# Kernel tuning notes

Hardware: AMD Instinct MI355X
Metric: run time of the kernel (lower is better)

## Reference

```python
import jax, jax.numpy as jnp
import numpy as np

I, H, B, T = 512, 1024, 64, 256

def _lstm_cell(x, h, c, Wih, Whh, bih, bhh):
    # PyTorch LSTMCell: gates ordered (i, f, g, o)
    g = x @ Wih.T + h @ Whh.T + (bih + bhh)
    i, f, gc, o = jnp.split(g, 4, axis=-1)
    i = jax.nn.sigmoid(i)
    f = jax.nn.sigmoid(f)
    gc = jnp.tanh(gc)
    o = jax.nn.sigmoid(o)
    c_new = f * c + i * gc
    return o * jnp.tanh(c_new), c_new

def setup_inputs() -> dict:
    key = jax.random.key(0)
    ks = jax.random.split(key, 20)
    s = 0.05
    d = {"x": jax.random.normal(ks[0], (B, T, I), dtype=jnp.float32)}
    # cell1: input I; cells 2-4: input H
    ins = [I, H, H, H]
    k = 1
    for n in range(1, 5):
        d[f"Wih{n}"] = jax.random.normal(ks[k], (4 * H, ins[n - 1]), dtype=jnp.float32) * s; k += 1
        d[f"Whh{n}"] = jax.random.normal(ks[k], (4 * H, H), dtype=jnp.float32) * s; k += 1
        d[f"bih{n}"] = jax.random.normal(ks[k], (4 * H,), dtype=jnp.float32) * s; k += 1
        d[f"bhh{n}"] = jax.random.normal(ks[k], (4 * H,), dtype=jnp.float32) * s; k += 1
    return d

def _mtrnn(x, Wih1, Whh1, bih1, bhh1, Wih2, Whh2, bih2, bhh2,
           Wih3, Whh3, bih3, bhh3, Wih4, Whh4, bih4, bhh4):
    b = x.shape[0]
    z = jnp.zeros((b, H), dtype=x.dtype)
    init = (z, z, z, z, z, z, z, z)

    def step(carry, inp):
        x_t, t = inp
        h1, c1, h2, c2, h3, c3, h4, c4 = carry
        h1, c1 = _lstm_cell(x_t, h1, c1, Wih1, Whh1, bih1, bhh1)
        nh2, nc2 = _lstm_cell(h1, h2, c2, Wih2, Whh2, bih2, bhh2)
        m2 = (t % 2 == 0)
        h2 = jnp.where(m2, nh2, h2); c2 = jnp.where(m2, nc2, c2)
        nh3, nc3 = _lstm_cell(h2, h3, c3, Wih3, Whh3, bih3, bhh3)
        m3 = (t % 4 == 0)
        h3 = jnp.where(m3, nh3, h3); c3 = jnp.where(m3, nc3, c3)
        nh4, nc4 = _lstm_cell(h3, h4, c4, Wih4, Whh4, bih4, bhh4)
        m4 = (t % 8 == 0)
        h4 = jnp.where(m4, nh4, h4); c4 = jnp.where(m4, nc4, c4)
        return (h1, c1, h2, c2, h3, c3, h4, c4), None

    xs = (jnp.transpose(x, (1, 0, 2)), jnp.arange(x.shape[1]))  # time-major scan
    (h1, c1, h2, c2, h3, c3, h4, c4), _ = jax.lax.scan(step, init, xs)
    return h4

def reference(x, Wih1, Whh1, bih1, bhh1, Wih2, Whh2, bih2, bhh2,
              Wih3, Whh3, bih3, bhh3, Wih4, Whh4, bih4, bhh4):
    return _mtrnn(x, Wih1, Whh1, bih1, bhh1, Wih2, Whh2, bih2, bhh2,
                  Wih3, Whh3, bih3, bhh3, Wih4, Whh4, bih4, bhh4)
```

## Files before the change

kernel.cpp:

```cpp
#include <hip/hip_runtime.h>

using u16 = unsigned short;
typedef short bf16x8 __attribute__((ext_vector_type(8)));
typedef float f32x4 __attribute__((ext_vector_type(4)));

static constexpr size_t OFF_W1  = 0;
static constexpr size_t OFF_W2  = OFF_W1 + (size_t)4096*1536*2;
static constexpr size_t OFF_W3  = OFF_W2 + (size_t)4096*2048*2;
static constexpr size_t OFF_W4  = OFF_W3 + (size_t)4096*2048*2;
static constexpr size_t OFF_BS  = OFF_W4 + (size_t)4096*2048*2;
static constexpr size_t OFF_XB  = OFF_BS + (size_t)4*4096*4;
static constexpr size_t OFF_H   = OFF_XB + (size_t)256*64*512*2;
static constexpr size_t OFF_C   = OFF_H  + (size_t)4*2*65536*2;
static constexpr size_t OFF_BAR = OFF_C  + (size_t)4*65536*4;
static constexpr size_t WS_TOTAL= OFF_BAR + 4096;

__device__ __forceinline__ u16 f2b(float f) {
  union { float f; unsigned u; } a; a.f = f;
  unsigned r = a.u + 0x7fffu + ((a.u >> 16) & 1u);
  return (u16)(r >> 16);
}

__global__ void k_prep_cell(const float* __restrict__ Wih, const float* __restrict__ Whh,
                            int Kih, int Khh, u16* __restrict__ Wcat)
{
  const int r = blockIdx.y;
  const int k = blockIdx.x * blockDim.x + threadIdx.x;
  const int K = Kih + Khh;
  float v = (k < Kih) ? Wih[(size_t)r * Kih + k] : Whh[(size_t)r * Khh + (k - Kih)];
  Wcat[(size_t)r * K + k] = f2b(v);
}

__global__ void k_bsum(const float* b1i, const float* b1h, const float* b2i, const float* b2h,
                       const float* b3i, const float* b3h, const float* b4i, const float* b4h,
                       float* __restrict__ bs)
{
  const int i = blockIdx.x * blockDim.x + threadIdx.x;
  const int n = i >> 12, j = i & 4095;
  const float* bi = (n == 0) ? b1i : (n == 1) ? b2i : (n == 2) ? b3i : b4i;
  const float* bh = (n == 0) ? b1h : (n == 1) ? b2h : (n == 2) ? b3h : b4h;
  bs[i] = bi[j] + bh[j];
}

__global__ void k_xconv(const float* __restrict__ x, u16* __restrict__ xb)
{
  const int blk = blockIdx.x;
  const int t = blk >> 6, b = blk & 63;
  const int i = threadIdx.x * 4;
  const float4 v = *(const float4*)(x + ((size_t)b * 256 + t) * 512 + i);
  ushort4 s;
  s.x = f2b(v.x); s.y = f2b(v.y); s.z = f2b(v.z); s.w = f2b(v.w);
  *(ushort4*)(xb + (size_t)blk * 512 + i) = s;
}

__global__ void k_zero(uint4* __restrict__ p, int n16)
{
  const int i = blockIdx.x * blockDim.x + threadIdx.x;
  if (i < n16) { uint4 z; z.x = z.y = z.z = z.w = 0u; p[i] = z; }
}

__device__ __forceinline__ void grid_barrier(unsigned* bar, unsigned gen)
{
  __syncthreads();
  if (threadIdx.x == 0) {
    unsigned* gcnt = bar + ((blockIdx.x & 7) << 5);
    unsigned* root = bar + 256;
    unsigned* rel  = bar + 288;
    const unsigned p = __hip_atomic_fetch_add(gcnt, 1u, __ATOMIC_ACQ_REL, __HIP_MEMORY_SCOPE_AGENT);
    if (p == gen * 16u + 15u) {
      const unsigned q = __hip_atomic_fetch_add(root, 1u, __ATOMIC_ACQ_REL, __HIP_MEMORY_SCOPE_AGENT);
      if (q == gen * 8u + 7u)
        __hip_atomic_store(rel, gen + 1u, __ATOMIC_RELEASE, __HIP_MEMORY_SCOPE_AGENT);
    }
    while (__hip_atomic_load(rel, __ATOMIC_ACQUIRE, __HIP_MEMORY_SCOPE_AGENT) < gen + 1u)
      __builtin_amdgcn_s_sleep(2);
  }
  __syncthreads();
}

template<int NSEC>
__device__ __forceinline__ void run_cell(
    char* A_lds, float (*gl)[32][17],
    const u16* const (&src)[NSEC], const int (&sstr)[NSEC], const int (&soff)[NSEC],
    const u16* __restrict__ Wc, const int Kw,
    const float* __restrict__ bsum, float* __restrict__ cst,
    u16* __restrict__ hnext, float* __restrict__ outp,
    const int rh, const int cg)
{
  const int tid  = threadIdx.x;
  const int lane = tid & 63;
  const int wv   = tid >> 6;
  const int l15  = lane & 15;
  const int l4   = lane >> 4;
  const int xr   = (l15 & 7) << 4;

  f32x4 acc0 = {0.f, 0.f, 0.f, 0.f};
  f32x4 acc1 = {0.f, 0.f, 0.f, 0.f};

  const size_t wrow = (size_t)((wv << 10) + (cg << 4) + l15) * (size_t)Kw + (l4 << 3);

  uint4 wA[16], wB[16];
  {
    const u16* wr = Wc + wrow;
    #pragma unroll
    for (int k0 = 0; k0 < 16; ++k0) wA[k0] = *(const uint4*)(wr + (k0 << 5));
  }

  #pragma unroll
  for (int s = 0; s < NSEC; ++s) {
    __syncthreads();
    {
      const u16* S = src[s];
      const int st = sstr[s];
      const int so = soff[s];
      #pragma unroll
      for (int i = 0; i < 8; ++i) {
        const int ch = tid + (i << 8);
        const int lr = ch >> 6;
        const int kc = (ch & 63) << 3;
        const uint4 v = *(const uint4*)(S + (size_t)(rh * 32 + lr) * st + so + kc);
        *(uint4*)(A_lds + lr * 1024 + ((kc * 2) ^ ((lr & 7) << 4))) = v;
      }
    }
    if (s + 1 < NSEC) {
      const u16* wr = Wc + wrow + ((s + 1) << 9);
      if ((s & 1) == 0) {
        #pragma unroll
        for (int k0 = 0; k0 < 16; ++k0) wB[k0] = *(const uint4*)(wr + (k0 << 5));
      } else {
        #pragma unroll
        for (int k0 = 0; k0 < 16; ++k0) wA[k0] = *(const uint4*)(wr + (k0 << 5));
      }
    }
    __syncthreads();
    const uint4* wc = ((s & 1) == 0) ? wA : wB;
    #pragma unroll
    for (int k0 = 0; k0 < 16; ++k0) {
      const int kb = (k0 << 6) + (l4 << 4);
      bf16x8 a0 = *(const bf16x8*)(A_lds + (l15 << 10) + (kb ^ xr));
      bf16x8 a1 = *(const bf16x8*)(A_lds + ((16 + l15) << 10) + (kb ^ xr));
      bf16x8 b  = __builtin_bit_cast(bf16x8, wc[k0]);
      acc0 = __builtin_amdgcn_mfma_f32_16x16x32_bf16(a0, b, acc0, 0, 0, 0);
      acc1 = __builtin_amdgcn_mfma_f32_16x16x32_bf16(a1, b, acc1, 0, 0, 0);
    }
  }

  __syncthreads();
  #pragma unroll
  for (int r = 0; r < 4; ++r) {
    gl[wv][(l4 << 2) + r][l15]      = acc0[r];
    gl[wv][16 + (l4 << 2) + r][l15] = acc1[r];
  }
  __syncthreads();

  for (int e = tid; e < 512; e += 256) {
    const int lr = e >> 4, lc = e & 15;
    const int col  = (cg << 4) + lc;
    const int brow = rh * 32 + lr;
    const float gi = gl[0][lr][lc] + bsum[col];
    const float gf = gl[1][lr][lc] + bsum[1024 + col];
    const float gg = gl[2][lr][lc] + bsum[2048 + col];
    const float go = gl[3][lr][lc] + bsum[3072 + col];
    const float ii = 1.f / (1.f + __expf(-gi));
    const float ff = 1.f / (1.f + __expf(-gf));
    const float gc = tanhf(gg);
    const float oo = 1.f / (1.f + __expf(-go));
    const int idx = (brow << 10) + col;
    const float cn = ff * cst[idx] + ii * gc;
    cst[idx] = cn;
    const float hn = oo * tanhf(cn);
    hnext[idx] = f2b(hn);
    if (outp) outp[idx] = hn;
  }
}

__global__ void __launch_bounds__(256) k_mtrnn(char* __restrict__ ws, float* __restrict__ out)
{
  __shared__ alignas(16) char A_lds[32768];
  __shared__ float gl[4][32][17];

  const int bid = blockIdx.x;
  const int rh  = bid & 1;
  const int cg  = bid >> 1;

  const u16* W1 = (const u16*)(ws + OFF_W1);
  const u16* W2 = (const u16*)(ws + OFF_W2);
  const u16* W3 = (const u16*)(ws + OFF_W3);
  const u16* W4 = (const u16*)(ws + OFF_W4);
  const float* bs = (const float*)(ws + OFF_BS);
  const u16* xb = (const u16*)(ws + OFF_XB);
  u16* hb       = (u16*)(ws + OFF_H);
  float* cs     = (float*)(ws + OFF_C);
  unsigned* bar = (unsigned*)(ws + OFF_BAR);

  #define HBUF(n, p) (hb + (((n) * 2 + (p)) << 16))

  unsigned gen = 0;
  int c1 = 0, c2 = 0, c3 = 0, c4 = 0;

  #pragma unroll 1
  for (int t = 0; t < 256; ++t) {
    {
      const u16* xt = xb + (size_t)t * 32768;
      const u16* h1 = HBUF(0, c1);
      const u16* src[3] = { xt, h1, h1 };
      const int sstr[3] = { 512, 1024, 1024 };
      const int soff[3] = { 0, 0, 512 };
      run_cell<3>(A_lds, gl, src, sstr, soff, W1, 1536, bs, cs,
                  HBUF(0, c1 ^ 1), nullptr, rh, cg);
      c1 ^= 1;
      grid_barrier(bar, gen); ++gen;
    }
    if ((t & 1) == 0) {
      const u16* hi = HBUF(0, c1);
      const u16* hs = HBUF(1, c2);
      const u16* src[4] = { hi, hi, hs, hs };
      const int sstr[4] = { 1024, 1024, 1024, 1024 };
      const int soff[4] = { 0, 512, 0, 512 };
      run_cell<4>(A_lds, gl, src, sstr, soff, W2, 2048, bs + 4096, cs + 65536,
                  HBUF(1, c2 ^ 1), nullptr, rh, cg);
      c2 ^= 1;
      grid_barrier(bar, gen); ++gen;
    }
    if ((t & 3) == 0) {
      const u16* hi = HBUF(1, c2);
      const u16* hs = HBUF(2, c3);
      const u16* src[4] = { hi, hi, hs, hs };
      const int sstr[4] = { 1024, 1024, 1024, 1024 };
      const int soff[4] = { 0, 512, 0, 512 };
      run_cell<4>(A_lds, gl, src, sstr, soff, W3, 2048, bs + 8192, cs + 131072,
                  HBUF(2, c3 ^ 1), nullptr, rh, cg);
      c3 ^= 1;
      grid_barrier(bar, gen); ++gen;
    }
    if ((t & 7) == 0) {
      const u16* hi = HBUF(2, c3);
      const u16* hs = HBUF(3, c4);
      const u16* src[4] = { hi, hi, hs, hs };
      const int sstr[4] = { 1024, 1024, 1024, 1024 };
      const int soff[4] = { 0, 512, 0, 512 };
      run_cell<4>(A_lds, gl, src, sstr, soff, W4, 2048, bs + 12288, cs + 196608,
                  HBUF(3, c4 ^ 1), out, rh, cg);
      c4 ^= 1;
      grid_barrier(bar, gen); ++gen;
    }
  }
  #undef HBUF
}

extern "C" void kernel_launch(void* const* d_in, const int* in_sizes, int n_in,
                              void* d_out, int out_size, void* d_ws, size_t ws_size,
                              hipStream_t stream)
{
  (void)in_sizes; (void)n_in; (void)out_size;
  if (ws_size < WS_TOTAL) return;

  const float* x = (const float*)d_in[0];
  const float* Wih[4] = { (const float*)d_in[1], (const float*)d_in[5],
                          (const float*)d_in[9], (const float*)d_in[13] };
  const float* Whh[4] = { (const float*)d_in[2], (const float*)d_in[6],
                          (const float*)d_in[10], (const float*)d_in[14] };
  const float* bih[4] = { (const float*)d_in[3], (const float*)d_in[7],
                          (const float*)d_in[11], (const float*)d_in[15] };
  const float* bhh[4] = { (const float*)d_in[4], (const float*)d_in[8],
                          (const float*)d_in[12], (const float*)d_in[16] };
  char* ws = (char*)d_ws;
  float* out = (float*)d_out;

  k_prep_cell<<<dim3(6, 4096), 256, 0, stream>>>(Wih[0], Whh[0], 512, 1024, (u16*)(ws + OFF_W1));
  k_prep_cell<<<dim3(8, 4096), 256, 0, stream>>>(Wih[1], Whh[1], 1024, 1024, (u16*)(ws + OFF_W2));
  k_prep_cell<<<dim3(8, 4096), 256, 0, stream>>>(Wih[2], Whh[2], 1024, 1024, (u16*)(ws + OFF_W3));
  k_prep_cell<<<dim3(8, 4096), 256, 0, stream>>>(Wih[3], Whh[3], 1024, 1024, (u16*)(ws + OFF_W4));
  k_bsum<<<64, 256, 0, stream>>>(bih[0], bhh[0], bih[1], bhh[1], bih[2], bhh[2], bih[3], bhh[3],
                                 (float*)(ws + OFF_BS));
  k_xconv<<<16384, 128, 0, stream>>>(x, (u16*)(ws + OFF_XB));
  {
    const int n16 = (int)((WS_TOTAL - OFF_H) / 16);
    k_zero<<<(n16 + 255) / 256, 256, 0, stream>>>((uint4*)(ws + OFF_H), n16);
  }
  k_mtrnn<<<128, 256, 0, stream>>>(ws, out);
}
```

Measured before the change: 10.95 ms.

## Keep per-cell weights resident in registers with cell-specialized persistent blocks

The persistent kernel now launches 256 blocks of 512 threads, each dedicated to one of the four cells and one 16-column group. Each block converts its slice of the weights from fp32 to bf16 once, straight from the inputs, and keeps it in registers, so no weight memory is streamed per timestep and the separate weight-prep kernels go away. The K dimension is split between two wave halves (input vs recurrent), with partial sums reduced through LDS. Risks include heavy register pressure (32 uint4 per thread), blocks for inactive cells sitting idle at every barrier, and each block now processing all 64 batch rows.

```diff
diff --git a/kernel.cpp b/kernel.cpp
--- a/kernel.cpp
+++ b/kernel.cpp
@@ -4,12 +4,8 @@
 typedef short bf16x8 __attribute__((ext_vector_type(8)));
 typedef float f32x4 __attribute__((ext_vector_type(4)));
 
-static constexpr size_t OFF_W1  = 0;
-static constexpr size_t OFF_W2  = OFF_W1 + (size_t)4096*1536*2;
-static constexpr size_t OFF_W3  = OFF_W2 + (size_t)4096*2048*2;
-static constexpr size_t OFF_W4  = OFF_W3 + (size_t)4096*2048*2;
-static constexpr size_t OFF_BS  = OFF_W4 + (size_t)4096*2048*2;
-static constexpr size_t OFF_XB  = OFF_BS + (size_t)4*4096*4;
+static constexpr size_t OFF_BS  = 0;
+static constexpr size_t OFF_XB  = 65536;
 static constexpr size_t OFF_H   = OFF_XB + (size_t)256*64*512*2;
 static constexpr size_t OFF_C   = OFF_H  + (size_t)4*2*65536*2;
 static constexpr size_t OFF_BAR = OFF_C  + (size_t)4*65536*4;
@@ -19,16 +15,6 @@
   union { float f; unsigned u; } a; a.f = f;
   unsigned r = a.u + 0x7fffu + ((a.u >> 16) & 1u);
   return (u16)(r >> 16);
-}
-
-__global__ void k_prep_cell(const float* __restrict__ Wih, const float* __restrict__ Whh,
-                            int Kih, int Khh, u16* __restrict__ Wcat)
-{
-  const int r = blockIdx.y;
-  const int k = blockIdx.x * blockDim.x + threadIdx.x;
-  const int K = Kih + Khh;
-  float v = (k < Kih) ? Wih[(size_t)r * Kih + k] : Whh[(size_t)r * Khh + (k - Kih)];
-  Wcat[(size_t)r * K + k] = f2b(v);
 }
 
 __global__ void k_bsum(const float* b1i, const float* b1h, const float* b2i, const float* b2h,
@@ -67,44 +53,31 @@
     unsigned* root = bar + 256;
     unsigned* rel  = bar + 288;
     const unsigned p = __hip_atomic_fetch_add(gcnt, 1u, __ATOMIC_ACQ_REL, __HIP_MEMORY_SCOPE_AGENT);
-    if (p == gen * 16u + 15u) {
+    if (p == gen * 32u + 31u) {
       const unsigned q = __hip_atomic_fetch_add(root, 1u, __ATOMIC_ACQ_REL, __HIP_MEMORY_SCOPE_AGENT);
       if (q == gen * 8u + 7u)
         __hip_atomic_store(rel, gen + 1u, __ATOMIC_RELEASE, __HIP_MEMORY_SCOPE_AGENT);
     }
     while (__hip_atomic_load(rel, __ATOMIC_ACQUIRE, __HIP_MEMORY_SCOPE_AGENT) < gen + 1u)
-      __builtin_amdgcn_s_sleep(2);
+      __builtin_amdgcn_s_sleep(8);
   }
   __syncthreads();
 }
 
-template<int NSEC>
-__device__ __forceinline__ void run_cell(
-    char* A_lds, float (*gl)[32][17],
+#define GLI(kh, g, row, col) ((((kh) * 4 + (g)) * 64 + (row)) * 17 + (col))
+
+template<int NSEC, int S0>
+__device__ __forceinline__ void run_phase(
+    char* __restrict__ A_lds, float* __restrict__ gl, const float* __restrict__ bias_lds,
     const u16* const (&src)[NSEC], const int (&sstr)[NSEC], const int (&soff)[NSEC],
-    const u16* __restrict__ Wc, const int Kw,
-    const float* __restrict__ bsum, float* __restrict__ cst,
-    u16* __restrict__ hnext, float* __restrict__ outp,
-    const int rh, const int cg)
-{
-  const int tid  = threadIdx.x;
-  const int lane = tid & 63;
-  const int wv   = tid >> 6;
-  const int l15  = lane & 15;
-  const int l4   = lane >> 4;
-  const int xr   = (l15 & 7) << 4;
-
-  f32x4 acc0 = {0.f, 0.f, 0.f, 0.f};
-  f32x4 acc1 = {0.f, 0.f, 0.f, 0.f};
-
-  const size_t wrow = (size_t)((wv << 10) + (cg << 4) + l15) * (size_t)Kw + (l4 << 3);
-
-  uint4 wA[16], wB[16];
-  {
-    const u16* wr = Wc + wrow;
-    #pragma unroll
-    for (int k0 = 0; k0 < 16; ++k0) wA[k0] = *(const uint4*)(wr + (k0 << 5));
-  }
+    const uint4 (&w)[32],
+    float* __restrict__ cst, u16* __restrict__ hnext, float* __restrict__ outp,
+    const int cg, const int tid, const int g, const int kh,
+    const int l15, const int l4, const int xr)
+{
+  f32x4 acc[4];
+  #pragma unroll
+  for (int mt = 0; mt < 4; ++mt) acc[mt] = f32x4{0.f, 0.f, 0.f, 0.f};
 
   #pragma unroll
   for (int s = 0; s < NSEC; ++s) {
@@ -115,57 +88,64 @@
       const int so = soff[s];
       #pragma unroll
       for (int i = 0; i < 8; ++i) {
-        const int ch = tid + (i << 8);
+        const int ch = tid + (i << 9);
         const int lr = ch >> 6;
         const int kc = (ch & 63) << 3;
-        const uint4 v = *(const uint4*)(S + (size_t)(rh * 32 + lr) * st + so + kc);
+        const uint4 v = *(const uint4*)(S + (size_t)lr * st + so + kc);
         *(uint4*)(A_lds + lr * 1024 + ((kc * 2) ^ ((lr & 7) << 4))) = v;
       }
     }
-    if (s + 1 < NSEC) {
-      const u16* wr = Wc + wrow + ((s + 1) << 9);
-      if ((s & 1) == 0) {
+    __syncthreads();
+    if (kh == 0) {
+      if (s < S0) {
         #pragma unroll
-        for (int k0 = 0; k0 < 16; ++k0) wB[k0] = *(const uint4*)(wr + (k0 << 5));
-      } else {
+        for (int k = 0; k < 16; ++k) {
+          const int kb = (k << 6) + (l4 << 4);
+          #pragma unroll
+          for (int mt = 0; mt < 4; ++mt) {
+            bf16x8 a = *(const bf16x8*)(A_lds + ((mt * 16 + l15) << 10) + (kb ^ xr));
+            acc[mt] = __builtin_amdgcn_mfma_f32_16x16x32_bf16(
+                a, __builtin_bit_cast(bf16x8, w[s * 16 + k]), acc[mt], 0, 0, 0);
+          }
+        }
+      }
+    } else {
+      if (s >= S0) {
         #pragma unroll
-        for (int k0 = 0; k0 < 16; ++k0) wA[k0] = *(const uint4*)(wr + (k0 << 5));
-      }
-    }
-    __syncthreads();
-    const uint4* wc = ((s & 1) == 0) ? wA : wB;
+        for (int k = 0; k < 16; ++k) {
+          const int kb = (k << 6) + (l4 << 4);
+          #pragma unroll
+          for (int mt = 0; mt < 4; ++mt) {
+            bf16x8 a = *(const bf16x8*)(A_lds + ((mt * 16 + l15) << 10) + (kb ^ xr));
+            acc[mt] = __builtin_amdgcn_mfma_f32_16x16x32_bf16(
+                a, __builtin_bit_cast(bf16x8, w[(s - S0) * 16 + k]), acc[mt], 0, 0, 0);
+          }
+        }
+      }
+    }
+  }
+
+  __syncthreads();
+  #pragma unroll
+  for (int mt = 0; mt < 4; ++mt)
     #pragma unroll
-    for (int k0 = 0; k0 < 16; ++k0) {
-      const int kb = (k0 << 6) + (l4 << 4);
-      bf16x8 a0 = *(const bf16x8*)(A_lds + (l15 << 10) + (kb ^ xr));
-      bf16x8 a1 = *(const bf16x8*)(A_lds + ((16 + l15) << 10) + (kb ^ xr));
-      bf16x8 b  = __builtin_bit_cast(bf16x8, wc[k0]);
-      acc0 = __builtin_amdgcn_mfma_f32_16x16x32_bf16(a0, b, acc0, 0, 0, 0);
-      acc1 = __builtin_amdgcn_mfma_f32_16x16x32_bf16(a1, b, acc1, 0, 0, 0);
-    }
-  }
-
+    for (int r = 0; r < 4; ++r)
+      gl[GLI(kh, g, mt * 16 + (l4 << 2) + r, l15)] = acc[mt][r];
   __syncthreads();
-  #pragma unroll
-  for (int r = 0; r < 4; ++r) {
-    gl[wv][(l4 << 2) + r][l15]      = acc0[r];
-    gl[wv][16 + (l4 << 2) + r][l15] = acc1[r];
-  }
-  __syncthreads();
-
-  for (int e = tid; e < 512; e += 256) {
-    const int lr = e >> 4, lc = e & 15;
-    const int col  = (cg << 4) + lc;
-    const int brow = rh * 32 + lr;
-    const float gi = gl[0][lr][lc] + bsum[col];
-    const float gf = gl[1][lr][lc] + bsum[1024 + col];
-    const float gg = gl[2][lr][lc] + bsum[2048 + col];
-    const float go = gl[3][lr][lc] + bsum[3072 + col];
+
+  #pragma unroll
+  for (int ee = 0; ee < 2; ++ee) {
+    const int e = tid + (ee << 9);
+    const int row = e >> 4, lc = e & 15;
+    const float gi = gl[GLI(0, 0, row, lc)] + gl[GLI(1, 0, row, lc)] + bias_lds[lc];
+    const float gf = gl[GLI(0, 1, row, lc)] + gl[GLI(1, 1, row, lc)] + bias_lds[16 + lc];
+    const float gg = gl[GLI(0, 2, row, lc)] + gl[GLI(1, 2, row, lc)] + bias_lds[32 + lc];
+    const float go = gl[GLI(0, 3, row, lc)] + gl[GLI(1, 3, row, lc)] + bias_lds[48 + lc];
     const float ii = 1.f / (1.f + __expf(-gi));
     const float ff = 1.f / (1.f + __expf(-gf));
     const float gc = tanhf(gg);
     const float oo = 1.f / (1.f + __expf(-go));
-    const int idx = (brow << 10) + col;
+    const int idx = (row << 10) + (cg << 4) + lc;
     const float cn = ff * cst[idx] + ii * gc;
     cst[idx] = cn;
     const float hn = oo * tanhf(cn);
@@ -174,25 +154,66 @@
   }
 }
 
-__global__ void __launch_bounds__(256) k_mtrnn(char* __restrict__ ws, float* __restrict__ out)
-{
-  __shared__ alignas(16) char A_lds[32768];
-  __shared__ float gl[4][32][17];
-
-  const int bid = blockIdx.x;
-  const int rh  = bid & 1;
-  const int cg  = bid >> 1;
-
-  const u16* W1 = (const u16*)(ws + OFF_W1);
-  const u16* W2 = (const u16*)(ws + OFF_W2);
-  const u16* W3 = (const u16*)(ws + OFF_W3);
-  const u16* W4 = (const u16*)(ws + OFF_W4);
+__global__ void __launch_bounds__(512, 2) k_mtrnn(
+    char* __restrict__ ws, float* __restrict__ out,
+    const float* __restrict__ w1i, const float* __restrict__ w1h,
+    const float* __restrict__ w2i, const float* __restrict__ w2h,
+    const float* __restrict__ w3i, const float* __restrict__ w3h,
+    const float* __restrict__ w4i, const float* __restrict__ w4h)
+{
+  __shared__ alignas(16) char A_lds[65536];
+  __shared__ float gl[2 * 4 * 64 * 17];
+  __shared__ float bias_lds[64];
+
+  const int bid  = blockIdx.x;
+  const int cell = bid >> 6;
+  const int cg   = bid & 63;
+  const int tid  = threadIdx.x;
+  const int lane = tid & 63;
+  const int wv   = tid >> 6;
+  const int g    = wv & 3;
+  const int kh   = wv >> 2;
+  const int l15  = lane & 15;
+  const int l4   = lane >> 4;
+  const int xr   = (l15 & 7) << 4;
+
   const float* bs = (const float*)(ws + OFF_BS);
   const u16* xb = (const u16*)(ws + OFF_XB);
   u16* hb       = (u16*)(ws + OFF_H);
   float* cs     = (float*)(ws + OFF_C);
   unsigned* bar = (unsigned*)(ws + OFF_BAR);
 
+  const float* wihp = (cell == 0) ? w1i : (cell == 1) ? w2i : (cell == 2) ? w3i : w4i;
+  const float* whhp = (cell == 0) ? w1h : (cell == 1) ? w2h : (cell == 2) ? w3h : w4h;
+  const int KIH = (cell == 0) ? 512 : 1024;
+  const float* wsrc = kh ? whhp : wihp;
+  const int Kw = kh ? 1024 : KIH;
+  const int NK = Kw >> 5;
+  const size_t wrowoff = (size_t)((g << 10) + (cg << 4) + l15) * (size_t)Kw + (l4 << 3);
+
+  uint4 w[32];
+  #pragma unroll
+  for (int ks = 0; ks < 32; ++ks) {
+    if (ks < NK) {
+      const float* p = wsrc + wrowoff + (ks << 5);
+      const float4 f0 = *(const float4*)(p);
+      const float4 f1 = *(const float4*)(p + 4);
+      uint4 v;
+      v.x = (unsigned)f2b(f0.x) | ((unsigned)f2b(f0.y) << 16);
+      v.y = (unsigned)f2b(f0.z) | ((unsigned)f2b(f0.w) << 16);
+      v.z = (unsigned)f2b(f1.x) | ((unsigned)f2b(f1.y) << 16);
+      v.w = (unsigned)f2b(f1.z) | ((unsigned)f2b(f1.w) << 16);
+      w[ks] = v;
+    }
+  }
+
+  if (tid < 64) {
+    const int bg = tid >> 4, bc = tid & 15;
+    bias_lds[tid] = bs[(cell << 12) + (bg << 10) + (cg << 4) + bc];
+  }
+
+  float* cst = cs + (cell << 16);
+
   #define HBUF(n, p) (hb + (((n) * 2 + (p)) << 16))
 
   unsigned gen = 0;
@@ -201,46 +222,53 @@
   #pragma unroll 1
   for (int t = 0; t < 256; ++t) {
     {
-      const u16* xt = xb + (size_t)t * 32768;
-      const u16* h1 = HBUF(0, c1);
-      const u16* src[3] = { xt, h1, h1 };
-      const int sstr[3] = { 512, 1024, 1024 };
-      const int soff[3] = { 0, 0, 512 };
-      run_cell<3>(A_lds, gl, src, sstr, soff, W1, 1536, bs, cs,
-                  HBUF(0, c1 ^ 1), nullptr, rh, cg);
+      if (cell == 0) {
+        const u16* h1 = HBUF(0, c1);
+        const u16* src[3] = { xb + (size_t)t * 32768, h1, h1 };
+        const int sstr[3] = { 512, 1024, 1024 };
+        const int soff[3] = { 0, 0, 512 };
+        run_phase<3, 1>(A_lds, gl, bias_lds, src, sstr, soff, w, cst,
+                        HBUF(0, c1 ^ 1), nullptr, cg, tid, g, kh, l15, l4, xr);
+      }
       c1 ^= 1;
       grid_barrier(bar, gen); ++gen;
     }
     if ((t & 1) == 0) {
-      const u16* hi = HBUF(0, c1);
-      const u16* hs = HBUF(1, c2);
-      const u16* src[4] = { hi, hi, hs, hs };
-      const int sstr[4] = { 1024, 1024, 1024, 1024 };
-      const int soff[4] = { 0, 512, 0, 512 };
-      run_cell<4>(A_lds, gl, src, sstr, soff, W2, 2048, bs + 4096, cs + 65536,
-                  HBUF(1, c2 ^ 1), nullptr, rh, cg);
+      if (cell == 1) {
+        const u16* hi = HBUF(0, c1);
+        const u16* hs = HBUF(1, c2);
+        const u16* src[4] = { hi, hi, hs, hs };
+        const int sstr[4] = { 1024, 1024, 1024, 1024 };
+        const int soff[4] = { 0, 512, 0, 512 };
+        run_phase<4, 2>(A_lds, gl, bias_lds, src, sstr, soff, w, cst,
+                        HBUF(1, c2 ^ 1), nullptr, cg, tid, g, kh, l15, l4, xr);
+      }
       c2 ^= 1;
       grid_barrier(bar, gen); ++gen;
     }
     if ((t & 3) == 0) {
-      const u16* hi = HBUF(1, c2);
-      const u16* hs = HBUF(2, c3);
-      const u16* src[4] = { hi, hi, hs, hs };
-      const int sstr[4] = { 1024, 1024, 1024, 1024 };
-      const int soff[4] = { 0, 512, 0, 512 };
-      run_cell<4>(A_lds, gl, src, sstr, soff, W3, 2048, bs + 8192, cs + 131072,
-                  HBUF(2, c3 ^ 1), nullptr, rh, cg);
+      if (cell == 2) {
+        const u16* hi = HBUF(1, c2);
+        const u16* hs = HBUF(2, c3);
+        const u16* src[4] = { hi, hi, hs, hs };
+        const int sstr[4] = { 1024, 1024, 1024, 1024 };
+        const int soff[4] = { 0, 512, 0, 512 };
+        run_phase<4, 2>(A_lds, gl, bias_lds, src, sstr, soff, w, cst,
+                        HBUF(2, c3 ^ 1), nullptr, cg, tid, g, kh, l15, l4, xr);
+      }
       c3 ^= 1;
       grid_barrier(bar, gen); ++gen;
     }
     if ((t & 7) == 0) {
-      const u16* hi = HBUF(2, c3);
-      const u16* hs = HBUF(3, c4);
-      const u16* src[4] = { hi, hi, hs, hs };
-      const int sstr[4] = { 1024, 1024, 1024, 1024 };
-      const int soff[4] = { 0, 512, 0, 512 };
-      run_cell<4>(A_lds, gl, src, sstr, soff, W4, 2048, bs + 12288, cs + 196608,
-                  HBUF(3, c4 ^ 1), out, rh, cg);
+      if (cell == 3) {
+        const u16* hi = HBUF(2, c3);
+        const u16* hs = HBUF(3, c4);
+        const u16* src[4] = { hi, hi, hs, hs };
+        const int sstr[4] = { 1024, 1024, 1024, 1024 };
+        const int soff[4] = { 0, 512, 0, 512 };
+        run_phase<4, 2>(A_lds, gl, bias_lds, src, sstr, soff, w, cst,
+                        HBUF(3, c4 ^ 1), out, cg, tid, g, kh, l15, l4, xr);
+      }
       c4 ^= 1;
       grid_barrier(bar, gen); ++gen;
     }
@@ -267,10 +295,6 @@
   char* ws = (char*)d_ws;
   float* out = (float*)d_out;
 
-  k_prep_cell<<<dim3(6, 4096), 256, 0, stream>>>(Wih[0], Whh[0], 512, 1024, (u16*)(ws + OFF_W1));
-  k_prep_cell<<<dim3(8, 4096), 256, 0, stream>>>(Wih[1], Whh[1], 1024, 1024, (u16*)(ws + OFF_W2));
-  k_prep_cell<<<dim3(8, 4096), 256, 0, stream>>>(Wih[2], Whh[2], 1024, 1024, (u16*)(ws + OFF_W3));
-  k_prep_cell<<<dim3(8, 4096), 256, 0, stream>>>(Wih[3], Whh[3], 1024, 1024, (u16*)(ws + OFF_W4));
   k_bsum<<<64, 256, 0, stream>>>(bih[0], bhh[0], bih[1], bhh[1], bih[2], bhh[2], bih[3], bhh[3],
                                  (float*)(ws + OFF_BS));
   k_xconv<<<16384, 128, 0, stream>>>(x, (u16*)(ws + OFF_XB));
@@ -278,5 +302,7 @@
     const int n16 = (int)((WS_TOTAL - OFF_H) / 16);
     k_zero<<<(n16 + 255) / 256, 256, 0, stream>>>((uint4*)(ws + OFF_H), n16);
   }
-  k_mtrnn<<<128, 256, 0, stream>>>(ws, out);
-}
+  k_mtrnn<<<256, 512, 0, stream>>>(ws, out,
+                                   Wih[0], Whh[0], Wih[1], Whh[1],
+                                   Wih[2], Whh[2], Wih[3], Whh[3]);
+}
```

Result: slower. 25.57 ms (+133.4%).
